# Kernel tuning notes

Hardware: AMD Instinct MI355X
Metric: run time of the kernel (lower is better)

## Reference

```python
import jax, jax.numpy as jnp
import numpy as np

B, C, H, W = 8, 512, 64, 64


def setup_inputs() -> dict:
    key = jax.random.key(0)
    k1, k2, k3, k4 = jax.random.split(key, 4)
    x = jax.random.normal(k1, (B, C, H, W), dtype=jnp.float32)
    spatial_feat = jax.random.normal(k2, (B, C, H, W), dtype=jnp.float32)
    multi_scale_feat = jax.random.normal(k3, (B, C, H, W), dtype=jnp.float32)
    scale = jnp.array(1.0, dtype=jnp.float32)  # nn.Parameter(torch.tensor(1.0))
    conv_w = jax.random.normal(k4, (C, C), dtype=jnp.float32) * 0.02  # 1x1 conv kernel [out,in]
    conv_b = jnp.zeros((C,), dtype=jnp.float32)
    return {"x": x, "spatial_feat": spatial_feat, "multi_scale_feat": multi_scale_feat,
            "scale": scale, "conv_w": conv_w, "conv_b": conv_b}


def reference(x, spatial_feat, multi_scale_feat, scale, conv_w, conv_b):
    Bq, Cq, Hq, Wq = x.shape
    L = Hq * Wq
    query = x.reshape(Bq, Cq, L)                                   # [B,C,L]
    kv = jnp.concatenate([spatial_feat.reshape(Bq, Cq, L),
                          multi_scale_feat.reshape(Bq, Cq, L)], axis=1)  # [B,2C,L]
    # attn = scale * L^-0.5 * (query @ kv^T), channel attention [B,C,2C]
    attn = jnp.einsum('bcl,bkl->bck', query, kv) * (scale * (float(L) ** -0.5))
    attn = jax.nn.softmax(attn, axis=-1)
    fused = jnp.einsum('bck,bkl->bcl', attn, kv).reshape(Bq, Cq, Hq, Wq)  # [B,C,H,W]
    out = jnp.einsum('oc,bchw->bohw', conv_w, fused) + conv_b[None, :, None, None]
    return out
```

## Files before the change

### kernel.cpp

```cpp
#include <hip/hip_runtime.h>

#define Bq   8
#define Cc   512
#define Ll   4096
#define KV2  1024
#define KS   4
#define KSL  (Ll / KS)

typedef _Float16 f16;
typedef __attribute__((ext_vector_type(4))) _Float16 f16x4;
typedef __attribute__((ext_vector_type(8))) _Float16 f16x8;
typedef __attribute__((ext_vector_type(4))) float    f32x4;

__global__ __launch_bounds__(256) void p_cvt(const float* __restrict__ in,
                                             f16* __restrict__ hi, int n4) {
    int i = blockIdx.x * 256 + threadIdx.x;
    if (i >= n4) return;
    float4 v = ((const float4*)in)[i];
    f16x4 hv; hv[0] = (f16)v.x; hv[1] = (f16)v.y; hv[2] = (f16)v.z; hv[3] = (f16)v.w;
    ((f16x4*)hi)[i] = hv;
}

__global__ __launch_bounds__(256) void p_split(const float* __restrict__ in,
                                               f16* __restrict__ hi,
                                               f16* __restrict__ lo, int n4) {
    int i = blockIdx.x * 256 + threadIdx.x;
    if (i >= n4) return;
    float4 v = ((const float4*)in)[i];
    f16 h0 = (f16)v.x, h1 = (f16)v.y, h2 = (f16)v.z, h3 = (f16)v.w;
    f16x4 hv; hv[0] = h0; hv[1] = h1; hv[2] = h2; hv[3] = h3;
    f16x4 lv;
    lv[0] = (f16)(v.x - (float)h0); lv[1] = (f16)(v.y - (float)h1);
    lv[2] = (f16)(v.z - (float)h2); lv[3] = (f16)(v.w - (float)h3);
    ((f16x4*)hi)[i] = hv;
    ((f16x4*)lo)[i] = lv;
}

__global__ __launch_bounds__(256) void p_kv(const float* __restrict__ sp,
                                            const float* __restrict__ ms,
                                            f16* __restrict__ kvhi,
                                            f16* __restrict__ kvt) {
    __shared__ float tile[64][65];
    const int b = blockIdx.z, c0 = blockIdx.y * 64, l0 = blockIdx.x * 64;
    const int t = threadIdx.x;
    const int r = t >> 2, q = t & 3;
    const float* src = (c0 + r < Cc)
        ? sp + ((size_t)b * Cc + c0 + r) * Ll
        : ms + ((size_t)b * Cc + (c0 + r - Cc)) * Ll;
    #pragma unroll
    for (int i = 0; i < 4; ++i) {
        int col = q * 16 + i * 4;
        float4 v = *(const float4*)(src + l0 + col);
        f16x4 hv; hv[0] = (f16)v.x; hv[1] = (f16)v.y; hv[2] = (f16)v.z; hv[3] = (f16)v.w;
        *(f16x4*)&kvhi[((size_t)b * KV2 + c0 + r) * Ll + l0 + col] = hv;
        tile[r][col] = v.x; tile[r][col + 1] = v.y;
        tile[r][col + 2] = v.z; tile[r][col + 3] = v.w;
    }
    __syncthreads();
    const int ln = t >> 3, q8 = t & 7;
    #pragma unroll
    for (int p = 0; p < 2; ++p) {
        const int l = ln + 32 * p;
        f16x8 o;
        #pragma unroll
        for (int j = 0; j < 8; ++j) o[j] = (f16)tile[q8 * 8 + j][l];
        *(f16x8*)&kvt[((size_t)b * Ll + l0 + l) * KV2 + c0 + q8 * 8] = o;
    }
}

__global__ __launch_bounds__(256, 2) void gemm_k1(const f16* __restrict__ Xhi,
                                                  const f16* __restrict__ kvhi,
                                                  const float* __restrict__ scale_ptr,
                                                  f16* __restrict__ attnP) {
    __shared__ __align__(16) f16 sAh[128][40];
    __shared__ __align__(16) f16 sBn[128][40];

    const int z = blockIdx.z, b = z >> 2, s = z & 3;
    const int m0 = blockIdx.y * 128, n0 = blockIdx.x * 128;
    const int t = threadIdx.x;
    const int row = t >> 1, h = t & 1;
    const int w = t >> 6, lane = t & 63, quad = lane >> 4, lr = lane & 15;
    const int wm = (w & 1) * 64, wn = (w >> 1) * 64;

    const f16* gA = Xhi  + ((size_t)b * Cc  + m0 + row) * Ll + s * KSL;
    const f16* gB = kvhi + ((size_t)b * KV2 + n0 + row) * Ll + s * KSL;

    f32x4 acc[4][4];
    #pragma unroll
    for (int i = 0; i < 4; ++i)
        #pragma unroll
        for (int j = 0; j < 4; ++j) {
            acc[i][j][0] = 0.f; acc[i][j][1] = 0.f;
            acc[i][j][2] = 0.f; acc[i][j][3] = 0.f;
        }

    f16x8 ra0 = *(const f16x8*)(gA + 8 * h);
    f16x8 ra1 = *(const f16x8*)(gA + 8 * h + 16);
    f16x8 rb0 = *(const f16x8*)(gB + 8 * h);
    f16x8 rb1 = *(const f16x8*)(gB + 8 * h + 16);

    for (int k0 = 0; k0 < KSL; k0 += 32) {
        __syncthreads();
        *(f16x8*)&sAh[row][8 * h]      = ra0;
        *(f16x8*)&sAh[row][8 * h + 16] = ra1;
        *(f16x8*)&sBn[row][8 * h]      = rb0;
        *(f16x8*)&sBn[row][8 * h + 16] = rb1;
        __syncthreads();
        if (k0 + 32 < KSL) {
            ra0 = *(const f16x8*)(gA + k0 + 32 + 8 * h);
            ra1 = *(const f16x8*)(gA + k0 + 32 + 8 * h + 16);
            rb0 = *(const f16x8*)(gB + k0 + 32 + 8 * h);
            rb1 = *(const f16x8*)(gB + k0 + 32 + 8 * h + 16);
        }
        f16x8 af[4], bf[4];
        #pragma unroll
        for (int i = 0; i < 4; ++i)
            af[i] = *(const f16x8*)&sAh[wm + i * 16 + lr][8 * quad];
        #pragma unroll
        for (int j = 0; j < 4; ++j)
            bf[j] = *(const f16x8*)&sBn[wn + j * 16 + lr][8 * quad];
        #pragma unroll
        for (int i = 0; i < 4; ++i)
            #pragma unroll
            for (int j = 0; j < 4; ++j)
                acc[i][j] = __builtin_amdgcn_mfma_f32_16x16x32_f16(af[i], bf[j], acc[i][j], 0, 0, 0);
    }

    const float alpha = scale_ptr[0] * 0.015625f;
    f16* Cs = attnP + (size_t)s * Bq * Cc * KV2 + (size_t)b * Cc * KV2;
    #pragma unroll
    for (int i = 0; i < 4; ++i)
        #pragma unroll
        for (int j = 0; j < 4; ++j) {
            const int n = n0 + wn + j * 16 + lr;
            #pragma unroll
            for (int r = 0; r < 4; ++r) {
                const int m = m0 + wm + i * 16 + quad * 4 + r;
                Cs[(size_t)m * KV2 + n] = (f16)(alpha * acc[i][j][r]);
            }
        }
}

__global__ __launch_bounds__(256) void k2_softmax_t(const f16* __restrict__ attnP,
                                                    f16* __restrict__ attnT) {
    __shared__ float rmax[16], rinv[16];
    __shared__ __align__(16) f16 tile[16][68];
    const int b = blockIdx.y, c0 = blockIdx.x * 16;
    const int t = threadIdx.x, w = t >> 6, lane = t & 63;
    const size_t sS = (size_t)Bq * Cc * KV2;

    for (int rr = 0; rr < 4; ++rr) {
        const int r = w * 4 + rr;
        const f16* base = attnP + ((size_t)b * Cc + c0 + r) * KV2;
        float v[16];
        #pragma unroll
        for (int i = 0; i < 2; ++i) {
            f16x8 u = *(const f16x8*)(base + (lane + 64 * i) * 8);
            #pragma unroll
            for (int j = 0; j < 8; ++j) v[i * 8 + j] = (float)u[j];
        }
        #pragma unroll
        for (int s = 1; s < KS; ++s) {
            const f16* bs = base + (size_t)s * sS;
            #pragma unroll
            for (int i = 0; i < 2; ++i) {
                f16x8 u = *(const f16x8*)(bs + (lane + 64 * i) * 8);
                #pragma unroll
                for (int j = 0; j < 8; ++j) v[i * 8 + j] += (float)u[j];
            }
        }
        float m = -3.4e38f;
        #pragma unroll
        for (int i = 0; i < 16; ++i) m = fmaxf(m, v[i]);
        #pragma unroll
        for (int off = 32; off; off >>= 1) m = fmaxf(m, __shfl_xor(m, off));
        float s = 0.f;
        #pragma unroll
        for (int i = 0; i < 16; ++i) s += __expf(v[i] - m);
        #pragma unroll
        for (int off = 32; off; off >>= 1) s += __shfl_xor(s, off);
        if (lane == 0) { rmax[r] = m; rinv[r] = 1.0f / s; }
    }
    __syncthreads();

    const int r2 = t >> 4, cn = (t & 15) * 4;
    const int n4 = t >> 2, q = t & 3;
    for (int nt = 0; nt < 16; ++nt) {
        const f16* base = attnP + ((size_t)b * Cc + c0 + r2) * KV2 + nt * 64 + cn;
        float vx[4];
        {
            f16x4 u = *(const f16x4*)base;
            #pragma unroll
            for (int j = 0; j < 4; ++j) vx[j] = (float)u[j];
        }
        #pragma unroll
        for (int s = 1; s < KS; ++s) {
            f16x4 u = *(const f16x4*)(base + (size_t)s * sS);
            #pragma unroll
            for (int j = 0; j < 4; ++j) vx[j] += (float)u[j];
        }
        const float m = rmax[r2], iv = rinv[r2];
        f16x4 hv;
        hv[0] = (f16)(__expf(vx[0] - m) * iv); hv[1] = (f16)(__expf(vx[1] - m) * iv);
        hv[2] = (f16)(__expf(vx[2] - m) * iv); hv[3] = (f16)(__expf(vx[3] - m) * iv);
        *(f16x4*)&tile[r2][cn] = hv;
        __syncthreads();
        f16x4 o;
        o[0] = tile[q * 4 + 0][n4]; o[1] = tile[q * 4 + 1][n4];
        o[2] = tile[q * 4 + 2][n4]; o[3] = tile[q * 4 + 3][n4];
        *(f16x4*)&attnT[((size_t)b * KV2 + nt * 64 + n4) * Cc + c0 + q * 4] = o;
        __syncthreads();
    }
}

template<int KD, int NC, int EPI, bool LO>
__global__ __launch_bounds__(256, 2) void gemm_nt(
    const f16* __restrict__ Ah, const f16* __restrict__ Al, size_t sA,
    const f16* __restrict__ Bh, size_t sB,
    const float* __restrict__ bias,
    float* __restrict__ Cf, f16* __restrict__ Chi, size_t sC) {
    __shared__ __align__(16) f16 sAh[128][40];
    __shared__ __align__(16) f16 sAl[LO ? 128 : 1][40];
    __shared__ __align__(16) f16 sBn[128][40];

    const int b = blockIdx.z, m0 = blockIdx.y * 128, n0 = blockIdx.x * 128;
    const int t = threadIdx.x;
    const int row = t >> 1, h = t & 1;
    const int w = t >> 6, lane = t & 63, quad = lane >> 4, lr = lane & 15;
    const int wm = (w & 1) * 64, wn = (w >> 1) * 64;

    const f16* gA  = Ah + b * sA + (size_t)(m0 + row) * KD;
    const f16* gAl = LO ? (Al + b * sA + (size_t)(m0 + row) * KD) : nullptr;
    const f16* gB  = Bh + b * sB + (size_t)(n0 + row) * KD;

    f32x4 acc[4][4];
    #pragma unroll
    for (int i = 0; i < 4; ++i)
        #pragma unroll
        for (int j = 0; j < 4; ++j) {
            acc[i][j][0] = 0.f; acc[i][j][1] = 0.f;
            acc[i][j][2] = 0.f; acc[i][j][3] = 0.f;
        }

    f16x8 ra0 = *(const f16x8*)(gA + 8 * h);
    f16x8 ra1 = *(const f16x8*)(gA + 8 * h + 16);
    f16x8 rl0, rl1;
    if constexpr (LO) {
        rl0 = *(const f16x8*)(gAl + 8 * h);
        rl1 = *(const f16x8*)(gAl + 8 * h + 16);
    }
    f16x8 rb0 = *(const f16x8*)(gB + 8 * h);
    f16x8 rb1 = *(const f16x8*)(gB + 8 * h + 16);

    for (int k0 = 0; k0 < KD; k0 += 32) {
        __syncthreads();
        *(f16x8*)&sAh[row][8 * h]      = ra0;
        *(f16x8*)&sAh[row][8 * h + 16] = ra1;
        if constexpr (LO) {
            *(f16x8*)&sAl[row][8 * h]      = rl0;
            *(f16x8*)&sAl[row][8 * h + 16] = rl1;
        }
        *(f16x8*)&sBn[row][8 * h]      = rb0;
        *(f16x8*)&sBn[row][8 * h + 16] = rb1;
        __syncthreads();
        if (k0 + 32 < KD) {
            ra0 = *(const f16x8*)(gA + k0 + 32 + 8 * h);
            ra1 = *(const f16x8*)(gA + k0 + 32 + 8 * h + 16);
            if constexpr (LO) {
                rl0 = *(const f16x8*)(gAl + k0 + 32 + 8 * h);
                rl1 = *(const f16x8*)(gAl + k0 + 32 + 8 * h + 16);
            }
            rb0 = *(const f16x8*)(gB + k0 + 32 + 8 * h);
            rb1 = *(const f16x8*)(gB + k0 + 32 + 8 * h + 16);
        }
        f16x8 af[4], alf[4], bf[4];
        #pragma unroll
        for (int i = 0; i < 4; ++i) {
            af[i] = *(const f16x8*)&sAh[wm + i * 16 + lr][8 * quad];
            if constexpr (LO) alf[i] = *(const f16x8*)&sAl[wm + i * 16 + lr][8 * quad];
        }
        #pragma unroll
        for (int j = 0; j < 4; ++j)
            bf[j] = *(const f16x8*)&sBn[wn + j * 16 + lr][8 * quad];
        #pragma unroll
        for (int i = 0; i < 4; ++i)
            #pragma unroll
            for (int j = 0; j < 4; ++j) {
                acc[i][j] = __builtin_amdgcn_mfma_f32_16x16x32_f16(af[i], bf[j], acc[i][j], 0, 0, 0);
                if constexpr (LO)
                    acc[i][j] = __builtin_amdgcn_mfma_f32_16x16x32_f16(alf[i], bf[j], acc[i][j], 0, 0, 0);
            }
    }

    #pragma unroll
    for (int i = 0; i < 4; ++i)
        #pragma unroll
        for (int j = 0; j < 4; ++j) {
            const int n = n0 + wn + j * 16 + lr;
            #pragma unroll
            for (int r = 0; r < 4; ++r) {
                const int m = m0 + wm + i * 16 + quad * 4 + r;
                const size_t idx = b * sC + (size_t)m * NC + n;
                const float v = acc[i][j][r];
                if constexpr (EPI == 1) Chi[idx] = (f16)v;
                else                    Cf[idx] = v + bias[m];
            }
        }
}

#define BM 64
#define BN 64
#define BK 32
#define PAD 4

__device__ __forceinline__ const float* kv_row(const float* __restrict__ sp,
                                               const float* __restrict__ ms,
                                               int b, int k) {
    return (k < Cc) ? (sp + ((size_t)b * Cc + k) * Ll)
                    : (ms + ((size_t)b * Cc + (k - Cc)) * Ll);
}

__global__ __launch_bounds__(256) void k1_logits(const float* __restrict__ x,
                                                 const float* __restrict__ sp,
                                                 const float* __restrict__ ms,
                                                 const float* __restrict__ scale,
                                                 float* __restrict__ attn) {
    __shared__ __align__(16) float As[BK][BM + PAD];
    __shared__ __align__(16) float Bs[BK][BN + PAD];
    const int b = blockIdx.z, m0 = blockIdx.y * BM, n0 = blockIdx.x * BN;
    const int t = threadIdx.x, tx = t & 15, ty = t >> 4, q = t & 7, r = t >> 3;
    const float alpha = scale[0] * (1.0f / 64.0f);
    const float* Abase = x + (size_t)b * Cc * Ll;
    float acc[4][4] = {};
    for (int k0 = 0; k0 < Ll; k0 += BK) {
        #pragma unroll
        for (int hh = 0; hh < 2; ++hh) {
            const int rw = r + 32 * hh;
            float4 v = *(const float4*)(Abase + (size_t)(m0 + rw) * Ll + k0 + 4 * q);
            As[4*q+0][rw] = v.x; As[4*q+1][rw] = v.y; As[4*q+2][rw] = v.z; As[4*q+3][rw] = v.w;
        }
        #pragma unroll
        for (int hh = 0; hh < 2; ++hh) {
            const int rw = r + 32 * hh;
            const float* Brow = kv_row(sp, ms, b, n0 + rw);
            float4 v = *(const float4*)(Brow + k0 + 4 * q);
            Bs[4*q+0][rw] = v.x; Bs[4*q+1][rw] = v.y; Bs[4*q+2][rw] = v.z; Bs[4*q+3][rw] = v.w;
        }
        __syncthreads();
        #pragma unroll
        for (int k = 0; k < BK; ++k) {
            float a[4], bb[4];
            *(float4*)a  = *(const float4*)&As[k][4 * ty];
            *(float4*)bb = *(const float4*)&Bs[k][4 * tx];
            #pragma unroll
            for (int i = 0; i < 4; ++i)
                #pragma unroll
                for (int j = 0; j < 4; ++j) acc[i][j] += a[i] * bb[j];
        }
        __syncthreads();
    }
    #pragma unroll
    for (int i = 0; i < 4; ++i) {
        const int m = m0 + 4 * ty + i;
        float4 o;
        o.x = alpha * acc[i][0]; o.y = alpha * acc[i][1];
        o.z = alpha * acc[i][2]; o.w = alpha * acc[i][3];
        *(float4*)(attn + ((size_t)b * Cc + m) * KV2 + n0 + 4 * tx) = o;
    }
}

__global__ __launch_bounds__(256) void k2_softmax(float* __restrict__ attn) {
    float* p = attn + (size_t)blockIdx.x * KV2;
    const int t = threadIdx.x, lane = t & 63, wv = t >> 6;
    float4 v = ((const float4*)p)[t];
    float m = fmaxf(fmaxf(v.x, v.y), fmaxf(v.z, v.w));
    #pragma unroll
    for (int off = 32; off; off >>= 1) m = fmaxf(m, __shfl_down(m, off));
    __shared__ float redm[4];
    if (lane == 0) redm[wv] = m;
    __syncthreads();
    m = fmaxf(fmaxf(redm[0], redm[1]), fmaxf(redm[2], redm[3]));
    v.x = __expf(v.x - m); v.y = __expf(v.y - m);
    v.z = __expf(v.z - m); v.w = __expf(v.w - m);
    float s = v.x + v.y + v.z + v.w;
    #pragma unroll
    for (int off = 32; off; off >>= 1) s += __shfl_down(s, off);
    __shared__ float reds[4];
    if (lane == 0) reds[wv] = s;
    __syncthreads();
    s = reds[0] + reds[1] + reds[2] + reds[3];
    const float inv = 1.0f / s;
    v.x *= inv; v.y *= inv; v.z *= inv; v.w *= inv;
    ((float4*)p)[t] = v;
}

__global__ __launch_bounds__(256) void k3_wattn(const float* __restrict__ W,
                                                const float* __restrict__ attn,
                                                float* __restrict__ attn2) {
    __shared__ __align__(16) float As[BK][BM + PAD];
    __shared__ __align__(16) float Bs[BK][BN];
    const int b = blockIdx.z, m0 = blockIdx.y * BM, n0 = blockIdx.x * BN;
    const int t = threadIdx.x, tx = t & 15, ty = t >> 4;
    const int q = t & 7, r = t >> 3, c4 = t & 15, kr = t >> 4;
    const float* Bbase = attn + (size_t)b * Cc * KV2;
    float acc[4][4] = {};
    for (int k0 = 0; k0 < Cc; k0 += BK) {
        #pragma unroll
        for (int hh = 0; hh < 2; ++hh) {
            const int rw = r + 32 * hh;
            float4 v = *(const float4*)(W + (size_t)(m0 + rw) * Cc + k0 + 4 * q);
            As[4*q+0][rw] = v.x; As[4*q+1][rw] = v.y; As[4*q+2][rw] = v.z; As[4*q+3][rw] = v.w;
        }
        #pragma unroll
        for (int hh = 0; hh < 2; ++hh) {
            const int k = kr + 16 * hh;
            float4 v = *(const float4*)(Bbase + (size_t)(k0 + k) * KV2 + n0 + 4 * c4);
            *(float4*)&Bs[k][4 * c4] = v;
        }
        __syncthreads();
        #pragma unroll
        for (int k = 0; k < BK; ++k) {
            float a[4], bb[4];
            *(float4*)a  = *(const float4*)&As[k][4 * ty];
            *(float4*)bb = *(const float4*)&Bs[k][4 * tx];
            #pragma unroll
            for (int i = 0; i < 4; ++i)
                #pragma unroll
                for (int j = 0; j < 4; ++j) acc[i][j] += a[i] * bb[j];
        }
        __syncthreads();
    }
    #pragma unroll
    for (int i = 0; i < 4; ++i) {
        const int m = m0 + 4 * ty + i;
        float4 o;
        o.x = acc[i][0]; o.y = acc[i][1]; o.z = acc[i][2]; o.w = acc[i][3];
        *(float4*)(attn2 + ((size_t)b * Cc + m) * KV2 + n0 + 4 * tx) = o;
    }
}

__global__ __launch_bounds__(256) void k4_out(const float* __restrict__ attn2,
                                              const float* __restrict__ sp,
                                              const float* __restrict__ ms,
                                              const float* __restrict__ bias,
                                              float* __restrict__ out) {
    __shared__ __align__(16) float As[BK][BM + PAD];
    __shared__ __align__(16) float Bs[BK][BN];
    const int b = blockIdx.z, m0 = blockIdx.y * BM, n0 = blockIdx.x * BN;
    const int t = threadIdx.x, tx = t & 15, ty = t >> 4;
    const int q = t & 7, r = t >> 3, c4 = t & 15, kr = t >> 4;
    const float* Abase = attn2 + (size_t)b * Cc * KV2;
    float acc[4][4] = {};
    for (int k0 = 0; k0 < KV2; k0 += BK) {
        #pragma unroll
        for (int hh = 0; hh < 2; ++hh) {
            const int rw = r + 32 * hh;
            float4 v = *(const float4*)(Abase + (size_t)(m0 + rw) * KV2 + k0 + 4 * q);
            As[4*q+0][rw] = v.x; As[4*q+1][rw] = v.y; As[4*q+2][rw] = v.z; As[4*q+3][rw] = v.w;
        }
        #pragma unroll
        for (int hh = 0; hh < 2; ++hh) {
            const int k = kr + 16 * hh;
            const float* Brow = kv_row(sp, ms, b, k0 + k);
            float4 v = *(const float4*)(Brow + n0 + 4 * c4);
            *(float4*)&Bs[k][4 * c4] = v;
        }
        __syncthreads();
        #pragma unroll
        for (int k = 0; k < BK; ++k) {
            float a[4], bb[4];
            *(float4*)a  = *(const float4*)&As[k][4 * ty];
            *(float4*)bb = *(const float4*)&Bs[k][4 * tx];
            #pragma unroll
            for (int i = 0; i < 4; ++i)
                #pragma unroll
                for (int j = 0; j < 4; ++j) acc[i][j] += a[i] * bb[j];
        }
        __syncthreads();
    }
    #pragma unroll
    for (int i = 0; i < 4; ++i) {
        const int m = m0 + 4 * ty + i;
        const float bm = bias[m];
        float4 o;
        o.x = acc[i][0] + bm; o.y = acc[i][1] + bm;
        o.z = acc[i][2] + bm; o.w = acc[i][3] + bm;
        *(float4*)(out + ((size_t)b * Cc + m) * Ll + n0 + 4 * tx) = o;
    }
}

extern "C" void kernel_launch(void* const* d_in, const int* in_sizes, int n_in,
                              void* d_out, int out_size, void* d_ws, size_t ws_size,
                              hipStream_t stream) {
    const float* x     = (const float*)d_in[0];
    const float* sp    = (const float*)d_in[1];
    const float* ms    = (const float*)d_in[2];
    const float* scale = (const float*)d_in[3];
    const float* W     = (const float*)d_in[4];
    const float* bias  = (const float*)d_in[5];
    float* out = (float*)d_out;

    const size_t NEED = 219152384;
    if (ws_size >= NEED) {
        char* ws = (char*)d_ws;
        f16* attnP = (f16*)ws;
        f16* Xhi   = (f16*)(ws + 33554432);
        f16* KVhi  = (f16*)(ws + 67108864);
        f16* KVT   = (f16*)(ws + 134217728);
        f16* Whi   = (f16*)(ws + 201326592);
        f16* Wlo   = (f16*)(ws + 201850880);
        f16* attnT = (f16*)(ws + 202375168);
        f16* A2hi  = (f16*)(ws + 210763776);

        dim3 blk(256);
        p_cvt  <<<dim3(16384),                 blk, 0, stream>>>(x, Xhi, Bq * Cc * Ll / 4);
        p_kv   <<<dim3(Ll / 64, KV2 / 64, Bq), blk, 0, stream>>>(sp, ms, KVhi, KVT);
        p_split<<<dim3(256),                   blk, 0, stream>>>(W, Whi, Wlo, Cc * Cc / 4);

        gemm_k1<<<dim3(KV2 / 128, Cc / 128, Bq * KS), blk, 0, stream>>>(Xhi, KVhi, scale, attnP);

        k2_softmax_t<<<dim3(Cc / 16, Bq), blk, 0, stream>>>(attnP, attnT);

        gemm_nt<Cc, KV2, 1, true><<<dim3(KV2 / 128, Cc / 128, Bq), blk, 0, stream>>>(
            Whi, Wlo, (size_t)0, attnT, (size_t)KV2 * Cc,
            nullptr, nullptr, A2hi, (size_t)Cc * KV2);

        gemm_nt<KV2, Ll, 2, false><<<dim3(Ll / 128, Cc / 128, Bq), blk, 0, stream>>>(
            A2hi, nullptr, (size_t)Cc * KV2, KVT, (size_t)Ll * KV2,
            bias, out, nullptr, (size_t)Cc * Ll);
    } else {
        float* attn  = (float*)d_ws;
        float* attn2 = attn + (size_t)Bq * Cc * KV2;
        dim3 blk(256);
        k1_logits <<<dim3(KV2 / BN, Cc / BM, Bq), blk, 0, stream>>>(x, sp, ms, scale, attn);
        k2_softmax<<<dim3(Bq * Cc),               blk, 0, stream>>>(attn);
        k3_wattn  <<<dim3(KV2 / BN, Cc / BM, Bq), blk, 0, stream>>>(W, attn, attn2);
        k4_out    <<<dim3(Ll / BN, Cc / BM, Bq), blk, 0, stream>>>(attn2, sp, ms, bias, out);
    }
}
```

Measured before the change: 390.5 us.

## Unify GEMMs into one MFMA kernel with direct global-to-LDS loads and swizzle

```diff
diff --git a/kernel.cpp b/kernel.cpp
--- a/kernel.cpp
+++ b/kernel.cpp
@@ -11,6 +11,13 @@
 typedef __attribute__((ext_vector_type(4))) _Float16 f16x4;
 typedef __attribute__((ext_vector_type(8))) _Float16 f16x8;
 typedef __attribute__((ext_vector_type(4))) float    f32x4;
+
+typedef const __attribute__((address_space(1))) void* gas_t;
+typedef __attribute__((address_space(3))) void*       las_t;
+
+__device__ __forceinline__ void gl16(const f16* g, f16* l) {
+    __builtin_amdgcn_global_load_lds((gas_t)g, (las_t)l, 16, 0, 0);
+}
 
 __global__ __launch_bounds__(256) void p_cvt(const float* __restrict__ in,
                                              f16* __restrict__ hi, int n4) {
@@ -68,22 +75,38 @@
     }
 }
 
-__global__ __launch_bounds__(256, 2) void gemm_k1(const f16* __restrict__ Xhi,
-                                                  const f16* __restrict__ kvhi,
-                                                  const float* __restrict__ scale_ptr,
-                                                  f16* __restrict__ attnP) {
-    __shared__ __align__(16) f16 sAh[128][40];
-    __shared__ __align__(16) f16 sBn[128][40];
-
-    const int z = blockIdx.z, b = z >> 2, s = z & 3;
-    const int m0 = blockIdx.y * 128, n0 = blockIdx.x * 128;
+template<int KD, int NBN, int EPI, bool LO, int KSV>
+__global__ __launch_bounds__(256, 3) void gemm_mfma(
+    const f16* __restrict__ Ah, const f16* __restrict__ Al, size_t sAb, int lda,
+    const f16* __restrict__ Bh, size_t sBb, int ldb,
+    const float* __restrict__ scale_ptr, const float* __restrict__ bias,
+    float* __restrict__ Cf, f16* __restrict__ Chi,
+    size_t sCb, size_t sliceC, int ldc)
+{
+    __shared__ __align__(16) f16 sA[128 * 64];
+    __shared__ __align__(16) f16 sB[128 * 64];
+    __shared__ __align__(16) f16 sL[LO ? 128 * 64 : 8];
+
+    int wg = blockIdx.x;
+    const int chunk = (int)gridDim.x >> 3;
+    wg = (wg & 7) * chunk + (wg >> 3);
+    const int m0 = (wg & 3) * 128; wg >>= 2;
+    const int n0 = (wg % NBN) * 128; wg /= NBN;
+    const int b  = wg / KSV, s = wg % KSV;
+
     const int t = threadIdx.x;
-    const int row = t >> 1, h = t & 1;
-    const int w = t >> 6, lane = t & 63, quad = lane >> 4, lr = lane & 15;
+    const int w = t >> 6, lane = t & 63;
+    const int quad = lane >> 4, lr = lane & 15;
     const int wm = (w & 1) * 64, wn = (w >> 1) * 64;
-
-    const f16* gA = Xhi  + ((size_t)b * Cc  + m0 + row) * Ll + s * KSL;
-    const f16* gB = kvhi + ((size_t)b * KV2 + n0 + row) * Ll + s * KSL;
+    const int sr = lane >> 3, sc = lane & 7;
+    const int swb = (sc ^ sr) << 3;
+    const int x7 = lr & 7;
+
+    const f16* gA = Ah + (size_t)b * sAb + (size_t)s * KD
+                  + (size_t)(m0 + w * 8 + sr) * lda + swb;
+    const f16* gB = Bh + (size_t)b * sBb + (size_t)s * KD
+                  + (size_t)(n0 + w * 8 + sr) * ldb + swb;
+    const f16* gL = LO ? (Al + (size_t)(m0 + w * 8 + sr) * lda + swb) : nullptr;
 
     f32x4 acc[4][4];
     #pragma unroll
@@ -94,51 +117,91 @@
             acc[i][j][2] = 0.f; acc[i][j][3] = 0.f;
         }
 
-    f16x8 ra0 = *(const f16x8*)(gA + 8 * h);
-    f16x8 ra1 = *(const f16x8*)(gA + 8 * h + 16);
-    f16x8 rb0 = *(const f16x8*)(gB + 8 * h);
-    f16x8 rb1 = *(const f16x8*)(gB + 8 * h + 16);
-
-    for (int k0 = 0; k0 < KSL; k0 += 32) {
-        __syncthreads();
-        *(f16x8*)&sAh[row][8 * h]      = ra0;
-        *(f16x8*)&sAh[row][8 * h + 16] = ra1;
-        *(f16x8*)&sBn[row][8 * h]      = rb0;
-        *(f16x8*)&sBn[row][8 * h + 16] = rb1;
-        __syncthreads();
-        if (k0 + 32 < KSL) {
-            ra0 = *(const f16x8*)(gA + k0 + 32 + 8 * h);
-            ra1 = *(const f16x8*)(gA + k0 + 32 + 8 * h + 16);
-            rb0 = *(const f16x8*)(gB + k0 + 32 + 8 * h);
-            rb1 = *(const f16x8*)(gB + k0 + 32 + 8 * h + 16);
-        }
-        f16x8 af[4], bf[4];
+    for (int k0 = 0; k0 < KD; k0 += 64) {
+        #pragma unroll
+        for (int i = 0; i < 4; ++i) {
+            gl16(gA + k0 + (size_t)(i * 32) * lda, &sA[(i * 32 + w * 8) * 64]);
+            gl16(gB + k0 + (size_t)(i * 32) * ldb, &sB[(i * 32 + w * 8) * 64]);
+            if constexpr (LO)
+                gl16(gL + k0 + (size_t)(i * 32) * lda, &sL[(i * 32 + w * 8) * 64]);
+        }
+        asm volatile("s_waitcnt vmcnt(0)" ::: "memory");
+        __syncthreads();
+        #pragma unroll
+        for (int ks = 0; ks < 2; ++ks) {
+            f16x8 af[4], bf[4];
+            #pragma unroll
+            for (int i = 0; i < 4; ++i)
+                af[i] = *(const f16x8*)&sA[(wm + i * 16 + lr) * 64
+                         + ((((ks << 2) | quad) ^ x7) << 3)];
+            #pragma unroll
+            for (int j = 0; j < 4; ++j)
+                bf[j] = *(const f16x8*)&sB[(wn + j * 16 + lr) * 64
+                         + ((((ks << 2) | quad) ^ x7) << 3)];
+            #pragma unroll
+            for (int i = 0; i < 4; ++i)
+                #pragma unroll
+                for (int j = 0; j < 4; ++j)
+                    acc[i][j] = __builtin_amdgcn_mfma_f32_16x16x32_f16(
+                                    af[i], bf[j], acc[i][j], 0, 0, 0);
+            if constexpr (LO) {
+                f16x8 lf[4];
+                #pragma unroll
+                for (int i = 0; i < 4; ++i)
+                    lf[i] = *(const f16x8*)&sL[(wm + i * 16 + lr) * 64
+                             + ((((ks << 2) | quad) ^ x7) << 3)];
+                #pragma unroll
+                for (int i = 0; i < 4; ++i)
+                    #pragma unroll
+                    for (int j = 0; j < 4; ++j)
+                        acc[i][j] = __builtin_amdgcn_mfma_f32_16x16x32_f16(
+                                        lf[i], bf[j], acc[i][j], 0, 0, 0);
+            }
+        }
+        __syncthreads();
+    }
+
+    if constexpr (EPI == 0) {
+        const float alpha = scale_ptr[0] * 0.015625f;
+        f16* Cs = Chi + (size_t)s * sliceC + (size_t)b * sCb;
         #pragma unroll
         for (int i = 0; i < 4; ++i)
-            af[i] = *(const f16x8*)&sAh[wm + i * 16 + lr][8 * quad];
-        #pragma unroll
-        for (int j = 0; j < 4; ++j)
-            bf[j] = *(const f16x8*)&sBn[wn + j * 16 + lr][8 * quad];
+            #pragma unroll
+            for (int j = 0; j < 4; ++j) {
+                const int n = n0 + wn + j * 16 + lr;
+                #pragma unroll
+                for (int r = 0; r < 4; ++r) {
+                    const int m = m0 + wm + i * 16 + quad * 4 + r;
+                    Cs[(size_t)m * ldc + n] = (f16)(alpha * acc[i][j][r]);
+                }
+            }
+    } else if constexpr (EPI == 1) {
+        f16* Cs = Chi + (size_t)b * sCb;
         #pragma unroll
         for (int i = 0; i < 4; ++i)
             #pragma unroll
-            for (int j = 0; j < 4; ++j)
-                acc[i][j] = __builtin_amdgcn_mfma_f32_16x16x32_f16(af[i], bf[j], acc[i][j], 0, 0, 0);
-    }
-
-    const float alpha = scale_ptr[0] * 0.015625f;
-    f16* Cs = attnP + (size_t)s * Bq * Cc * KV2 + (size_t)b * Cc * KV2;
-    #pragma unroll
-    for (int i = 0; i < 4; ++i)
-        #pragma unroll
-        for (int j = 0; j < 4; ++j) {
-            const int n = n0 + wn + j * 16 + lr;
-            #pragma unroll
-            for (int r = 0; r < 4; ++r) {
-                const int m = m0 + wm + i * 16 + quad * 4 + r;
-                Cs[(size_t)m * KV2 + n] = (f16)(alpha * acc[i][j][r]);
+            for (int j = 0; j < 4; ++j) {
+                const int n = n0 + wn + j * 16 + lr;
+                #pragma unroll
+                for (int r = 0; r < 4; ++r) {
+                    const int m = m0 + wm + i * 16 + quad * 4 + r;
+                    Cs[(size_t)m * ldc + n] = (f16)acc[i][j][r];
+                }
             }
-        }
+    } else {
+        float* Co = Cf + (size_t)b * sCb;
+        #pragma unroll
+        for (int i = 0; i < 4; ++i)
+            #pragma unroll
+            for (int j = 0; j < 4; ++j) {
+                const int n = n0 + wn + j * 16 + lr;
+                #pragma unroll
+                for (int r = 0; r < 4; ++r) {
+                    const int m = m0 + wm + i * 16 + quad * 4 + r;
+                    Co[(size_t)m * ldc + n] = acc[i][j][r] + bias[m];
+                }
+            }
+    }
 }
 
 __global__ __launch_bounds__(256) void k2_softmax_t(const f16* __restrict__ attnP,
@@ -211,101 +274,6 @@
         *(f16x4*)&attnT[((size_t)b * KV2 + nt * 64 + n4) * Cc + c0 + q * 4] = o;
         __syncthreads();
     }
-}
-
-template<int KD, int NC, int EPI, bool LO>
-__global__ __launch_bounds__(256, 2) void gemm_nt(
-    const f16* __restrict__ Ah, const f16* __restrict__ Al, size_t sA,
-    const f16* __restrict__ Bh, size_t sB,
-    const float* __restrict__ bias,
-    float* __restrict__ Cf, f16* __restrict__ Chi, size_t sC) {
-    __shared__ __align__(16) f16 sAh[128][40];
-    __shared__ __align__(16) f16 sAl[LO ? 128 : 1][40];
-    __shared__ __align__(16) f16 sBn[128][40];
-
-    const int b = blockIdx.z, m0 = blockIdx.y * 128, n0 = blockIdx.x * 128;
-    const int t = threadIdx.x;
-    const int row = t >> 1, h = t & 1;
-    const int w = t >> 6, lane = t & 63, quad = lane >> 4, lr = lane & 15;
-    const int wm = (w & 1) * 64, wn = (w >> 1) * 64;
-
-    const f16* gA  = Ah + b * sA + (size_t)(m0 + row) * KD;
-    const f16* gAl = LO ? (Al + b * sA + (size_t)(m0 + row) * KD) : nullptr;
-    const f16* gB  = Bh + b * sB + (size_t)(n0 + row) * KD;
-
-    f32x4 acc[4][4];
-    #pragma unroll
-    for (int i = 0; i < 4; ++i)
-        #pragma unroll
-        for (int j = 0; j < 4; ++j) {
-            acc[i][j][0] = 0.f; acc[i][j][1] = 0.f;
-            acc[i][j][2] = 0.f; acc[i][j][3] = 0.f;
-        }
-
-    f16x8 ra0 = *(const f16x8*)(gA + 8 * h);
-    f16x8 ra1 = *(const f16x8*)(gA + 8 * h + 16);
-    f16x8 rl0, rl1;
-    if constexpr (LO) {
-        rl0 = *(const f16x8*)(gAl + 8 * h);
-        rl1 = *(const f16x8*)(gAl + 8 * h + 16);
-    }
-    f16x8 rb0 = *(const f16x8*)(gB + 8 * h);
-    f16x8 rb1 = *(const f16x8*)(gB + 8 * h + 16);
-
-    for (int k0 = 0; k0 < KD; k0 += 32) {
-        __syncthreads();
-        *(f16x8*)&sAh[row][8 * h]      = ra0;
-        *(f16x8*)&sAh[row][8 * h + 16] = ra1;
-        if constexpr (LO) {
-            *(f16x8*)&sAl[row][8 * h]      = rl0;
-            *(f16x8*)&sAl[row][8 * h + 16] = rl1;
-        }
-        *(f16x8*)&sBn[row][8 * h]      = rb0;
-        *(f16x8*)&sBn[row][8 * h + 16] = rb1;
-        __syncthreads();
-        if (k0 + 32 < KD) {
-            ra0 = *(const f16x8*)(gA + k0 + 32 + 8 * h);
-            ra1 = *(const f16x8*)(gA + k0 + 32 + 8 * h + 16);
-            if constexpr (LO) {
-                rl0 = *(const f16x8*)(gAl + k0 + 32 + 8 * h);
-                rl1 = *(const f16x8*)(gAl + k0 + 32 + 8 * h + 16);
-            }
-            rb0 = *(const f16x8*)(gB + k0 + 32 + 8 * h);
-            rb1 = *(const f16x8*)(gB + k0 + 32 + 8 * h + 16);
-        }
-        f16x8 af[4], alf[4], bf[4];
-        #pragma unroll
-        for (int i = 0; i < 4; ++i) {
-            af[i] = *(const f16x8*)&sAh[wm + i * 16 + lr][8 * quad];
-            if constexpr (LO) alf[i] = *(const f16x8*)&sAl[wm + i * 16 + lr][8 * quad];
-        }
-        #pragma unroll
-        for (int j = 0; j < 4; ++j)
-            bf[j] = *(const f16x8*)&sBn[wn + j * 16 + lr][8 * quad];
-        #pragma unroll
-        for (int i = 0; i < 4; ++i)
-            #pragma unroll
-            for (int j = 0; j < 4; ++j) {
-                acc[i][j] = __builtin_amdgcn_mfma_f32_16x16x32_f16(af[i], bf[j], acc[i][j], 0, 0, 0);
-                if constexpr (LO)
-                    acc[i][j] = __builtin_amdgcn_mfma_f32_16x16x32_f16(alf[i], bf[j], acc[i][j], 0, 0, 0);
-            }
-    }
-
-    #pragma unroll
-    for (int i = 0; i < 4; ++i)
-        #pragma unroll
-        for (int j = 0; j < 4; ++j) {
-            const int n = n0 + wn + j * 16 + lr;
-            #pragma unroll
-            for (int r = 0; r < 4; ++r) {
-                const int m = m0 + wm + i * 16 + quad * 4 + r;
-                const size_t idx = b * sC + (size_t)m * NC + n;
-                const float v = acc[i][j][r];
-                if constexpr (EPI == 1) Chi[idx] = (f16)v;
-                else                    Cf[idx] = v + bias[m];
-            }
-        }
 }
 
 #define BM 64
@@ -517,17 +485,28 @@
         p_kv   <<<dim3(Ll / 64, KV2 / 64, Bq), blk, 0, stream>>>(sp, ms, KVhi, KVT);
         p_split<<<dim3(256),                   blk, 0, stream>>>(W, Whi, Wlo, Cc * Cc / 4);
 
-        gemm_k1<<<dim3(KV2 / 128, Cc / 128, Bq * KS), blk, 0, stream>>>(Xhi, KVhi, scale, attnP);
+        gemm_mfma<KSL, KV2 / 128, 0, false, KS>
+            <<<dim3(4 * (KV2 / 128) * Bq * KS), blk, 0, stream>>>(
+            Xhi, nullptr, (size_t)Cc * Ll, Ll,
+            KVhi, (size_t)KV2 * Ll, Ll,
+            scale, nullptr, nullptr, attnP,
+            (size_t)Cc * KV2, (size_t)Bq * Cc * KV2, KV2);
 
         k2_softmax_t<<<dim3(Cc / 16, Bq), blk, 0, stream>>>(attnP, attnT);
 
-        gemm_nt<Cc, KV2, 1, true><<<dim3(KV2 / 128, Cc / 128, Bq), blk, 0, stream>>>(
-            Whi, Wlo, (size_t)0, attnT, (size_t)KV2 * Cc,
-            nullptr, nullptr, A2hi, (size_t)Cc * KV2);
-
-        gemm_nt<KV2, Ll, 2, false><<<dim3(Ll / 128, Cc / 128, Bq), blk, 0, stream>>>(
-            A2hi, nullptr, (size_t)Cc * KV2, KVT, (size_t)Ll * KV2,
-            bias, out, nullptr, (size_t)Cc * Ll);
+        gemm_mfma<Cc, KV2 / 128, 1, true, 1>
+            <<<dim3(4 * (KV2 / 128) * Bq), blk, 0, stream>>>(
+            Whi, Wlo, (size_t)0, Cc,
+            attnT, (size_t)KV2 * Cc, Cc,
+            nullptr, nullptr, nullptr, A2hi,
+            (size_t)Cc * KV2, (size_t)0, KV2);
+
+        gemm_mfma<KV2, Ll / 128, 2, false, 1>
+            <<<dim3(4 * (Ll / 128) * Bq), blk, 0, stream>>>(
+            A2hi, nullptr, (size_t)Cc * KV2, KV2,
+            KVT, (size_t)Ll * KV2, KV2,
+            nullptr, bias, out, nullptr,
+            (size_t)Cc * Ll, (size_t)0, Ll);
     } else {
         float* attn  = (float*)d_ws;
         float* attn2 = attn + (size_t)Bq * Cc * KV2;
```

Measured after the change: 381.4 us. 2.3% less time.
